# Kernel tuning notes

Measured on AMD Instinct MI355X. Metric: run time of the kernel, lower is better.

## Reference

```python
import jax, jax.numpy as jnp
import numpy as np
import math

BSZ, SEQLEN, DIM = 16, 1, 4096
N_HEADS, N_KV_HEADS = 32, 8
HEAD_DIM = DIM // N_HEADS  # 128
MAX_SEQ_LEN = 4096
START_POS = 4095


def setup_inputs() -> dict:
    key = jax.random.key(0)
    ks = jax.random.split(key, 8)
    w_scale = 0.02
    x = jax.random.normal(ks[0], (1, BSZ, SEQLEN, DIM), jnp.float32)
    wq = jax.random.normal(ks[1], (DIM, DIM), jnp.float32) * w_scale
    wk = jax.random.normal(ks[2], (N_KV_HEADS * HEAD_DIM, DIM), jnp.float32) * w_scale
    wv = jax.random.normal(ks[3], (N_KV_HEADS * HEAD_DIM, DIM), jnp.float32) * w_scale
    wo = jax.random.normal(ks[4], (DIM, DIM), jnp.float32) * w_scale
    cache_k = jax.random.normal(ks[5], (BSZ, MAX_SEQ_LEN, N_KV_HEADS, HEAD_DIM), jnp.float32)
    cache_v = jax.random.normal(ks[6], (BSZ, MAX_SEQ_LEN, N_KV_HEADS, HEAD_DIM), jnp.float32)
    # real RoPE frequencies for positions [START_POS, START_POS+SEQLEN)
    inv_freq = 1.0 / (10000.0 ** (np.arange(0, HEAD_DIM, 2, dtype=np.float32) / HEAD_DIM))
    pos = np.arange(START_POS, START_POS + SEQLEN, dtype=np.float32)
    ang = pos[:, None] * inv_freq[None, :]  # [seqlen, head_dim/2]
    freqs_cos = jnp.asarray(np.cos(ang), jnp.float32)
    freqs_sin = jnp.asarray(np.sin(ang), jnp.float32)
    return {"x": x, "wq": wq, "wk": wk, "wv": wv, "wo": wo,
            "cache_k": cache_k, "cache_v": cache_v,
            "freqs_cos": freqs_cos, "freqs_sin": freqs_sin,
            "start_pos": START_POS}


def _apply_rope(t, cos, sin):
    # t: [b, s, h, d]; cos/sin: [s, d/2]; complex mult over interleaved pairs
    b, s, h, d = t.shape
    tr = t.reshape(b, s, h, d // 2, 2)
    a, bb = tr[..., 0], tr[..., 1]
    c = cos[None, :, None, :]
    sn = sin[None, :, None, :]
    out = jnp.stack([a * c - bb * sn, a * sn + bb * c], axis=-1)
    return out.reshape(b, s, h, d)


def reference(x, wq, wk, wv, wo, cache_k, cache_v, freqs_cos, freqs_sin, start_pos):
    _, bsz, seqlen, dim = x.shape
    n_kv_heads, head_dim = cache_k.shape[2], cache_k.shape[3]
    n_heads = dim // head_dim
    n_rep = n_heads // n_kv_heads

    xq = jnp.einsum('obsd,ed->obse', x, wq).reshape(bsz, seqlen, n_heads, head_dim)
    xk = jnp.einsum('obsd,ed->obse', x, wk).reshape(bsz, seqlen, n_kv_heads, head_dim)
    xv = jnp.einsum('obsd,ed->obse', x, wv).reshape(bsz, seqlen, n_kv_heads, head_dim)

    xq = _apply_rope(xq, freqs_cos, freqs_sin)
    xk = _apply_rope(xk, freqs_cos, freqs_sin)

    cache_k = cache_k.at[:, start_pos:start_pos + seqlen].set(xk)
    cache_v = cache_v.at[:, start_pos:start_pos + seqlen].set(xv)
    keys = cache_k[:, :start_pos + seqlen]    # [b, L, kvh, hd]
    values = cache_v[:, :start_pos + seqlen]

    # repeat_kv (GQA expansion)
    keys = jnp.repeat(keys, n_rep, axis=2)     # [b, L, h, hd]
    values = jnp.repeat(values, n_rep, axis=2)

    scale = 1.0 / math.sqrt(head_dim)
    scores = jnp.einsum('bqhd,bkhd->bhqk', xq, keys) * scale
    # mask is None in decode (seqlen == 1)
    attn = jax.nn.softmax(scores, axis=-1)
    out = jnp.einsum('bhqk,bkhd->bqhd', attn, values)
    out = out.reshape(1, bsz, seqlen, dim)
    return jnp.einsum('obsd,ed->obse', out, wo)
```

## Files before the change

### kernel.cpp

```cpp
#include <hip/hip_runtime.h>
#include <math.h>

#define BSZ 16
#define DIMM 4096
#define NKVH 8
#define HD 128
#define SEQ 4096
#define NSPLIT 16
#define SPLITLEN 256
#define RPAD 65

__device__ __forceinline__ void gll16(const float* src, float* dst) {
  __builtin_amdgcn_global_load_lds(
      (const __attribute__((address_space(1))) void*)src,
      (__attribute__((address_space(3))) void*)dst, 16, 0, 0);
}

__device__ __forceinline__ void stage_chunk(const float* __restrict__ xg,
                                            float* __restrict__ buf, int c,
                                            int wave, int lane) {
#pragma unroll
  for (int u = 0; u < 4; ++u) {
    gll16(xg + (size_t)(u * 4 + wave) * DIMM + c * 256 + (lane << 2),
          buf + u * 1024 + wave * 256);
  }
}

__device__ __forceinline__ void gemv_rows4(const float* __restrict__ xg,
                                           const float* __restrict__ W,
                                           int rbase,
                                           float* __restrict__ x_lds,
                                           float* __restrict__ rbuf,
                                           float res[4], int tid) {
  const int lane = tid & 63;
  const int wave = tid >> 6;
  float acc[4][16];
#pragma unroll
  for (int r = 0; r < 4; ++r)
#pragma unroll
    for (int b = 0; b < 16; ++b) acc[r][b] = 0.f;

  stage_chunk(xg, x_lds, 0, wave, lane);
  float4 w4[4];
#pragma unroll
  for (int r = 0; r < 4; ++r)
    w4[r] = *(const float4*)(W + (size_t)(rbase + r) * DIMM + (lane << 2));

  for (int c = 0; c < 16; ++c) {
    __syncthreads();
    float4 wn[4];
    if (c < 15) {
      stage_chunk(xg, x_lds + ((c + 1) & 1) * 4096, c + 1, wave, lane);
#pragma unroll
      for (int r = 0; r < 4; ++r)
        wn[r] = *(const float4*)(W + (size_t)(rbase + r) * DIMM +
                                 (c + 1) * 256 + (lane << 2));
    }
    const float4* xb = (const float4*)(x_lds + (c & 1) * 4096);
#pragma unroll
    for (int b = 0; b < 16; ++b) {
      float4 xv = xb[b * 64 + lane];
#pragma unroll
      for (int r = 0; r < 4; ++r) {
        acc[r][b] = fmaf(w4[r].x, xv.x, acc[r][b]);
        acc[r][b] = fmaf(w4[r].y, xv.y, acc[r][b]);
        acc[r][b] = fmaf(w4[r].z, xv.z, acc[r][b]);
        acc[r][b] = fmaf(w4[r].w, xv.w, acc[r][b]);
      }
    }
    if (c < 15) {
#pragma unroll
      for (int r = 0; r < 4; ++r) w4[r] = wn[r];
    }
  }

#pragma unroll
  for (int r = 0; r < 4; ++r) {
    __syncthreads();
#pragma unroll
    for (int b = 0; b < 16; ++b) rbuf[b * RPAD + lane] = acc[r][b];
    __syncthreads();
    int bb = lane >> 2, j = lane & 3;
    float s = 0.f;
#pragma unroll
    for (int k = 0; k < 16; ++k) s += rbuf[bb * RPAD + j * 16 + k];
    s += __shfl_xor(s, 1);
    s += __shfl_xor(s, 2);
    res[r] = s;
  }
}

__global__ __launch_bounds__(256) void qkv_kernel(
    const float* __restrict__ x, const float* __restrict__ wq,
    const float* __restrict__ wk, const float* __restrict__ wv,
    const float* __restrict__ fcos, const float* __restrict__ fsin,
    float* __restrict__ q_ws, float* __restrict__ k_ws,
    float* __restrict__ v_ws) {
  __shared__ float x_lds[2 * 4096];
  __shared__ float red[4][16 * RPAD];
  const int tid = threadIdx.x;
  const int lane = tid & 63;
  const int wave = tid >> 6;
  const int row0 = blockIdx.x * 16 + wave * 4;

  const float* W;
  int rbase, kind;
  if (row0 < 4096)      { W = wq; rbase = row0;        kind = 0; }
  else if (row0 < 5120) { W = wk; rbase = row0 - 4096; kind = 1; }
  else                  { W = wv; rbase = row0 - 5120; kind = 2; }

  float res[4];
  gemv_rows4(x, W, rbase, x_lds, red[wave], res, tid);

  if (kind <= 1) {
#pragma unroll
    for (int pr = 0; pr < 2; ++pr) {
      int i = ((rbase + pr * 2) & 127) >> 1;
      float c = fcos[i], s = fsin[i];
      float a = res[pr * 2], b2 = res[pr * 2 + 1];
      res[pr * 2]     = a * c - b2 * s;
      res[pr * 2 + 1] = a * s + b2 * c;
    }
  }
  if ((lane & 3) == 0) {
    int b = lane >> 2;
    if (kind == 0) {
#pragma unroll
      for (int r = 0; r < 4; ++r) q_ws[(size_t)b * 4096 + rbase + r] = res[r];
    } else {
      int kvh = rbase >> 7, dpos = rbase & 127;
      float* dst = (kind == 1) ? k_ws : v_ws;
#pragma unroll
      for (int r = 0; r < 4; ++r)
        dst[((size_t)b * NKVH + kvh) * HD + dpos + r] = res[r];
    }
  }
}

__global__ __launch_bounds__(256) void attn_kernel(
    const float* __restrict__ ck, const float* __restrict__ cv,
    const float* __restrict__ q_ws, const float* __restrict__ k_ws,
    const float* __restrict__ v_ws, float* __restrict__ ml_ws,
    float* __restrict__ opart) {
  __shared__ float sc[SPLITLEN * 4];
  __shared__ float part[32 * 128];
  const int tid = threadIdx.x, lane = tid & 63, wave = tid >> 6;
  const int split = blockIdx.x, kvh = blockIdx.y, b = blockIdx.z;
  const int p0 = split * SPLITLEN;
  const float scale = 0.08838834764831845f;

  {
    const int dsub = (lane & 7) << 2;
    const int prow = lane >> 3;
    float4 q4[4][4];
#pragma unroll
    for (int h = 0; h < 4; ++h)
#pragma unroll
      for (int j = 0; j < 4; ++j) {
        float4 t = *(const float4*)(q_ws + (size_t)b * 4096 + (kvh * 4 + h) * 128 + j * 32 + dsub);
        q4[h][j] = make_float4(t.x * scale, t.y * scale, t.z * scale, t.w * scale);
      }
#pragma unroll 2
    for (int it = 0; it < 8; ++it) {
      int pl = wave * 64 + it * 8 + prow;
      const float* kp = (p0 + pl == SEQ - 1)
                            ? (k_ws + ((size_t)b * NKVH + kvh) * HD)
                            : (ck + ((size_t)(b * 4096 + p0 + pl) * 8 + kvh) * 128);
      float s0 = 0, s1 = 0, s2 = 0, s3 = 0;
#pragma unroll
      for (int j = 0; j < 4; ++j) {
        float4 k4 = *(const float4*)(kp + j * 32 + dsub);
        s0 = fmaf(k4.x, q4[0][j].x, s0); s0 = fmaf(k4.y, q4[0][j].y, s0);
        s0 = fmaf(k4.z, q4[0][j].z, s0); s0 = fmaf(k4.w, q4[0][j].w, s0);
        s1 = fmaf(k4.x, q4[1][j].x, s1); s1 = fmaf(k4.y, q4[1][j].y, s1);
        s1 = fmaf(k4.z, q4[1][j].z, s1); s1 = fmaf(k4.w, q4[1][j].w, s1);
        s2 = fmaf(k4.x, q4[2][j].x, s2); s2 = fmaf(k4.y, q4[2][j].y, s2);
        s2 = fmaf(k4.z, q4[2][j].z, s2); s2 = fmaf(k4.w, q4[2][j].w, s2);
        s3 = fmaf(k4.x, q4[3][j].x, s3); s3 = fmaf(k4.y, q4[3][j].y, s3);
        s3 = fmaf(k4.z, q4[3][j].z, s3); s3 = fmaf(k4.w, q4[3][j].w, s3);
      }
#pragma unroll
      for (int m = 1; m <= 4; m <<= 1) {
        s0 += __shfl_xor(s0, m); s1 += __shfl_xor(s1, m);
        s2 += __shfl_xor(s2, m); s3 += __shfl_xor(s3, m);
      }
      if ((lane & 7) == 0)
        ((float4*)sc)[pl] = make_float4(s0, s1, s2, s3);
    }
  }
  __syncthreads();

  {
    int h = wave;
    float vals[4];
    float m = -1e30f;
#pragma unroll
    for (int k = 0; k < 4; ++k) {
      vals[k] = sc[(k * 64 + lane) * 4 + h];
      m = fmaxf(m, vals[k]);
    }
#pragma unroll
    for (int mk = 1; mk <= 32; mk <<= 1) m = fmaxf(m, __shfl_xor(m, mk));
    float lsum = 0;
#pragma unroll
    for (int k = 0; k < 4; ++k) {
      float e = __expf(vals[k] - m);
      sc[(k * 64 + lane) * 4 + h] = e;
      lsum += e;
    }
#pragma unroll
    for (int mk = 1; mk <= 32; mk <<= 1) lsum += __shfl_xor(lsum, mk);
    if (lane == 0) {
      int hg = kvh * 4 + h;
      ml_ws[((size_t)(b * 32 + hg) * NSPLIT + split) * 2 + 0] = m;
      ml_ws[((size_t)(b * 32 + hg) * NSPLIT + split) * 2 + 1] = lsum;
    }
  }
  __syncthreads();

  {
    const int dq = lane & 31;
    const int half = lane >> 5;
    float4 a0 = {0,0,0,0}, a1 = {0,0,0,0}, a2 = {0,0,0,0}, a3 = {0,0,0,0};
#pragma unroll 4
    for (int it = 0; it < 32; ++it) {
      int pl = wave * 64 + it * 2 + half;
      const float* vp = (p0 + pl == SEQ - 1)
                            ? (v_ws + ((size_t)b * NKVH + kvh) * HD)
                            : (cv + ((size_t)(b * 4096 + p0 + pl) * 8 + kvh) * 128);
      float4 v4 = *(const float4*)(vp + dq * 4);
      float4 s4 = ((const float4*)sc)[pl];
      a0.x = fmaf(s4.x, v4.x, a0.x); a0.y = fmaf(s4.x, v4.y, a0.y);
      a0.z = fmaf(s4.x, v4.z, a0.z); a0.w = fmaf(s4.x, v4.w, a0.w);
      a1.x = fmaf(s4.y, v4.x, a1.x); a1.y = fmaf(s4.y, v4.y, a1.y);
      a1.z = fmaf(s4.y, v4.z, a1.z); a1.w = fmaf(s4.y, v4.w, a1.w);
      a2.x = fmaf(s4.z, v4.x, a2.x); a2.y = fmaf(s4.z, v4.y, a2.y);
      a2.z = fmaf(s4.z, v4.z, a2.z); a2.w = fmaf(s4.z, v4.w, a2.w);
      a3.x = fmaf(s4.w, v4.x, a3.x); a3.y = fmaf(s4.w, v4.y, a3.y);
      a3.z = fmaf(s4.w, v4.z, a3.z); a3.w = fmaf(s4.w, v4.w, a3.w);
    }
    int rb = (half * 16 + wave * 4) * 128 + dq * 4;
    *(float4*)&part[rb + 0 * 128] = a0;
    *(float4*)&part[rb + 1 * 128] = a1;
    *(float4*)&part[rb + 2 * 128] = a2;
    *(float4*)&part[rb + 3 * 128] = a3;
  }
  __syncthreads();
  {
    int hh = tid >> 6, dd = (tid & 63) * 2;
    float o0 = 0, o1 = 0;
#pragma unroll
    for (int g = 0; g < 8; ++g) {
      int row = (g >> 2) * 16 + (g & 3) * 4 + hh;
      float2 p2 = *(const float2*)&part[row * 128 + dd];
      o0 += p2.x; o1 += p2.y;
    }
    int hg = kvh * 4 + hh;
    size_t base = ((size_t)(b * 32 + hg) * NSPLIT + split) * 128;
    *(float2*)(opart + base + dd) = make_float2(o0, o1);
  }
}

__global__ __launch_bounds__(128) void combine_kernel(
    const float* __restrict__ ml_ws, const float* __restrict__ opart,
    float* __restrict__ attn_ws) {
  int bh = blockIdx.x;
  int d = threadIdx.x;
  float mv[NSPLIT], lv[NSPLIT];
  float M = -1e30f;
#pragma unroll
  for (int i = 0; i < NSPLIT; ++i) {
    mv[i] = ml_ws[((size_t)bh * NSPLIT + i) * 2];
    lv[i] = ml_ws[((size_t)bh * NSPLIT + i) * 2 + 1];
    M = fmaxf(M, mv[i]);
  }
  float L = 0, o = 0;
#pragma unroll
  for (int i = 0; i < NSPLIT; ++i) {
    float w = __expf(mv[i] - M);
    L += w * lv[i];
    o += w * opart[((size_t)bh * NSPLIT + i) * 128 + d];
  }
  attn_ws[(size_t)bh * 128 + d] = o / L;
}

__global__ __launch_bounds__(256) void oproj_kernel(
    const float* __restrict__ xin, const float* __restrict__ wo,
    float* __restrict__ out) {
  __shared__ float x_lds[2 * 4096];
  __shared__ float red[4][16 * RPAD];
  const int tid = threadIdx.x;
  const int lane = tid & 63;
  const int wave = tid >> 6;
  const int row0 = blockIdx.x * 16 + wave * 4;
  float res[4];
  gemv_rows4(xin, wo, row0, x_lds, red[wave], res, tid);
  if ((lane & 3) == 0) {
    int b = lane >> 2;
#pragma unroll
    for (int r = 0; r < 4; ++r) out[(size_t)b * 4096 + row0 + r] = res[r];
  }
}

extern "C" void kernel_launch(void* const* d_in, const int* in_sizes, int n_in,
                              void* d_out, int out_size, void* d_ws, size_t ws_size,
                              hipStream_t stream) {
  const float* x  = (const float*)d_in[0];
  const float* wq = (const float*)d_in[1];
  const float* wk = (const float*)d_in[2];
  const float* wv = (const float*)d_in[3];
  const float* wo = (const float*)d_in[4];
  const float* ck = (const float*)d_in[5];
  const float* cv = (const float*)d_in[6];
  const float* fc = (const float*)d_in[7];
  const float* fs = (const float*)d_in[8];

  float* ws      = (float*)d_ws;
  float* q_ws    = ws;
  float* k_ws    = q_ws + 65536;
  float* v_ws    = k_ws + 16384;
  float* ml_ws   = v_ws + 16384;
  float* opart   = ml_ws + 16384;
  float* attn_ws = opart + 1048576;

  qkv_kernel<<<384, 256, 0, stream>>>(x, wq, wk, wv, fc, fs, q_ws, k_ws, v_ws);
  attn_kernel<<<dim3(NSPLIT, NKVH, BSZ), 256, 0, stream>>>(ck, cv, q_ws, k_ws, v_ws,
                                                           ml_ws, opart);
  combine_kernel<<<BSZ * 32, 128, 0, stream>>>(ml_ws, opart, attn_ws);
  oproj_kernel<<<256, 256, 0, stream>>>(attn_ws, wo, (float*)d_out);
}
```

Measured before the change: 632.7 us.

## Drop LDS staging in GEMV, use nontemporal loads, double attention splits

The GEMV helper no longer stages x through LDS with global_load_lds and block barriers. Each wave now reads x directly from global memory, relying on L1/L2 caching, and streams weights with nontemporal loads. The attention kernel doubles the number of splits (NSPLIT 32, SPLITLEN 128) to launch more blocks and uses nontemporal loads for the KV cache; the workspace offsets grow to match. The trade-off is more redundant global reads of x per wave and a larger combine step, in exchange for fewer barriers, no LDS footprint for x, and more parallelism in attention.

Result: faster. 615.2 us (-2.8%).

```diff
diff --git a/kernel.cpp b/kernel.cpp
--- a/kernel.cpp
+++ b/kernel.cpp
@@ -6,67 +6,55 @@
 #define NKVH 8
 #define HD 128
 #define SEQ 4096
-#define NSPLIT 16
-#define SPLITLEN 256
+#define NSPLIT 32
+#define SPLITLEN 128
 #define RPAD 65
 
-__device__ __forceinline__ void gll16(const float* src, float* dst) {
-  __builtin_amdgcn_global_load_lds(
-      (const __attribute__((address_space(1))) void*)src,
-      (__attribute__((address_space(3))) void*)dst, 16, 0, 0);
-}
-
-__device__ __forceinline__ void stage_chunk(const float* __restrict__ xg,
-                                            float* __restrict__ buf, int c,
-                                            int wave, int lane) {
-#pragma unroll
-  for (int u = 0; u < 4; ++u) {
-    gll16(xg + (size_t)(u * 4 + wave) * DIMM + c * 256 + (lane << 2),
-          buf + u * 1024 + wave * 256);
-  }
-}
-
-__device__ __forceinline__ void gemv_rows4(const float* __restrict__ xg,
-                                           const float* __restrict__ W,
-                                           int rbase,
-                                           float* __restrict__ x_lds,
-                                           float* __restrict__ rbuf,
-                                           float res[4], int tid) {
-  const int lane = tid & 63;
-  const int wave = tid >> 6;
+typedef float v4f __attribute__((ext_vector_type(4)));
+
+__device__ __forceinline__ v4f ldg4(const float* p) { return *(const v4f*)p; }
+__device__ __forceinline__ v4f ldnt4(const float* p) {
+  return __builtin_nontemporal_load((const v4f*)p);
+}
+
+__device__ __forceinline__ void gemv4_direct(const float* __restrict__ xg,
+                                             const float* __restrict__ W,
+                                             int rbase,
+                                             float* __restrict__ rbuf,
+                                             float res[4], int lane) {
   float acc[4][16];
 #pragma unroll
   for (int r = 0; r < 4; ++r)
 #pragma unroll
     for (int b = 0; b < 16; ++b) acc[r][b] = 0.f;
 
-  stage_chunk(xg, x_lds, 0, wave, lane);
-  float4 w4[4];
-#pragma unroll
-  for (int r = 0; r < 4; ++r)
-    w4[r] = *(const float4*)(W + (size_t)(rbase + r) * DIMM + (lane << 2));
+  const float* wbase = W + (size_t)rbase * DIMM + (lane << 2);
+  const float* xbase = xg + (lane << 2);
+
+  v4f w4[4];
+#pragma unroll
+  for (int r = 0; r < 4; ++r) w4[r] = ldnt4(wbase + (size_t)r * DIMM);
 
   for (int c = 0; c < 16; ++c) {
-    __syncthreads();
-    float4 wn[4];
+    v4f wn[4];
     if (c < 15) {
-      stage_chunk(xg, x_lds + ((c + 1) & 1) * 4096, c + 1, wave, lane);
 #pragma unroll
       for (int r = 0; r < 4; ++r)
-        wn[r] = *(const float4*)(W + (size_t)(rbase + r) * DIMM +
-                                 (c + 1) * 256 + (lane << 2));
-    }
-    const float4* xb = (const float4*)(x_lds + (c & 1) * 4096);
-#pragma unroll
-    for (int b = 0; b < 16; ++b) {
-      float4 xv = xb[b * 64 + lane];
-#pragma unroll
-      for (int r = 0; r < 4; ++r) {
-        acc[r][b] = fmaf(w4[r].x, xv.x, acc[r][b]);
-        acc[r][b] = fmaf(w4[r].y, xv.y, acc[r][b]);
-        acc[r][b] = fmaf(w4[r].z, xv.z, acc[r][b]);
-        acc[r][b] = fmaf(w4[r].w, xv.w, acc[r][b]);
-      }
+        wn[r] = ldnt4(wbase + (size_t)r * DIMM + (c + 1) * 256);
+    }
+#pragma unroll
+    for (int bh = 0; bh < 2; ++bh) {
+      v4f xv[8];
+#pragma unroll
+      for (int b = 0; b < 8; ++b)
+        xv[b] = ldg4(xbase + (size_t)(bh * 8 + b) * DIMM + c * 256);
+#pragma unroll
+      for (int b = 0; b < 8; ++b)
+#pragma unroll
+        for (int r = 0; r < 4; ++r)
+#pragma unroll
+          for (int e = 0; e < 4; ++e)
+            acc[r][bh * 8 + b] = fmaf(w4[r][e], xv[b][e], acc[r][bh * 8 + b]);
     }
     if (c < 15) {
 #pragma unroll
@@ -76,10 +64,8 @@
 
 #pragma unroll
   for (int r = 0; r < 4; ++r) {
-    __syncthreads();
 #pragma unroll
     for (int b = 0; b < 16; ++b) rbuf[b * RPAD + lane] = acc[r][b];
-    __syncthreads();
     int bb = lane >> 2, j = lane & 3;
     float s = 0.f;
 #pragma unroll
@@ -96,7 +82,6 @@
     const float* __restrict__ fcos, const float* __restrict__ fsin,
     float* __restrict__ q_ws, float* __restrict__ k_ws,
     float* __restrict__ v_ws) {
-  __shared__ float x_lds[2 * 4096];
   __shared__ float red[4][16 * RPAD];
   const int tid = threadIdx.x;
   const int lane = tid & 63;
@@ -110,7 +95,7 @@
   else                  { W = wv; rbase = row0 - 5120; kind = 2; }
 
   float res[4];
-  gemv_rows4(x, W, rbase, x_lds, red[wave], res, tid);
+  gemv4_direct(x, W, rbase, red[wave], res, lane);
 
   if (kind <= 1) {
 #pragma unroll
@@ -161,23 +146,23 @@
         q4[h][j] = make_float4(t.x * scale, t.y * scale, t.z * scale, t.w * scale);
       }
 #pragma unroll 2
-    for (int it = 0; it < 8; ++it) {
-      int pl = wave * 64 + it * 8 + prow;
+    for (int it = 0; it < SPLITLEN / 32; ++it) {
+      int pl = wave * (SPLITLEN / 4) + it * 8 + prow;
       const float* kp = (p0 + pl == SEQ - 1)
                             ? (k_ws + ((size_t)b * NKVH + kvh) * HD)
                             : (ck + ((size_t)(b * 4096 + p0 + pl) * 8 + kvh) * 128);
       float s0 = 0, s1 = 0, s2 = 0, s3 = 0;
 #pragma unroll
       for (int j = 0; j < 4; ++j) {
-        float4 k4 = *(const float4*)(kp + j * 32 + dsub);
-        s0 = fmaf(k4.x, q4[0][j].x, s0); s0 = fmaf(k4.y, q4[0][j].y, s0);
-        s0 = fmaf(k4.z, q4[0][j].z, s0); s0 = fmaf(k4.w, q4[0][j].w, s0);
-        s1 = fmaf(k4.x, q4[1][j].x, s1); s1 = fmaf(k4.y, q4[1][j].y, s1);
-        s1 = fmaf(k4.z, q4[1][j].z, s1); s1 = fmaf(k4.w, q4[1][j].w, s1);
-        s2 = fmaf(k4.x, q4[2][j].x, s2); s2 = fmaf(k4.y, q4[2][j].y, s2);
-        s2 = fmaf(k4.z, q4[2][j].z, s2); s2 = fmaf(k4.w, q4[2][j].w, s2);
-        s3 = fmaf(k4.x, q4[3][j].x, s3); s3 = fmaf(k4.y, q4[3][j].y, s3);
-        s3 = fmaf(k4.z, q4[3][j].z, s3); s3 = fmaf(k4.w, q4[3][j].w, s3);
+        v4f k4 = ldnt4(kp + j * 32 + dsub);
+        s0 = fmaf(k4[0], q4[0][j].x, s0); s0 = fmaf(k4[1], q4[0][j].y, s0);
+        s0 = fmaf(k4[2], q4[0][j].z, s0); s0 = fmaf(k4[3], q4[0][j].w, s0);
+        s1 = fmaf(k4[0], q4[1][j].x, s1); s1 = fmaf(k4[1], q4[1][j].y, s1);
+        s1 = fmaf(k4[2], q4[1][j].z, s1); s1 = fmaf(k4[3], q4[1][j].w, s1);
+        s2 = fmaf(k4[0], q4[2][j].x, s2); s2 = fmaf(k4[1], q4[2][j].y, s2);
+        s2 = fmaf(k4[2], q4[2][j].z, s2); s2 = fmaf(k4[3], q4[2][j].w, s2);
+        s3 = fmaf(k4[0], q4[3][j].x, s3); s3 = fmaf(k4[1], q4[3][j].y, s3);
+        s3 = fmaf(k4[2], q4[3][j].z, s3); s3 = fmaf(k4[3], q4[3][j].w, s3);
       }
 #pragma unroll
       for (int m = 1; m <= 4; m <<= 1) {
@@ -192,10 +177,10 @@
 
   {
     int h = wave;
-    float vals[4];
+    float vals[SPLITLEN / 64];
     float m = -1e30f;
 #pragma unroll
-    for (int k = 0; k < 4; ++k) {
+    for (int k = 0; k < SPLITLEN / 64; ++k) {
       vals[k] = sc[(k * 64 + lane) * 4 + h];
       m = fmaxf(m, vals[k]);
     }
@@ -203,7 +188,7 @@
     for (int mk = 1; mk <= 32; mk <<= 1) m = fmaxf(m, __shfl_xor(m, mk));
     float lsum = 0;
 #pragma unroll
-    for (int k = 0; k < 4; ++k) {
+    for (int k = 0; k < SPLITLEN / 64; ++k) {
       float e = __expf(vals[k] - m);
       sc[(k * 64 + lane) * 4 + h] = e;
       lsum += e;
@@ -223,21 +208,21 @@
     const int half = lane >> 5;
     float4 a0 = {0,0,0,0}, a1 = {0,0,0,0}, a2 = {0,0,0,0}, a3 = {0,0,0,0};
 #pragma unroll 4
-    for (int it = 0; it < 32; ++it) {
-      int pl = wave * 64 + it * 2 + half;
+    for (int it = 0; it < SPLITLEN / 8; ++it) {
+      int pl = wave * (SPLITLEN / 4) + it * 2 + half;
       const float* vp = (p0 + pl == SEQ - 1)
                             ? (v_ws + ((size_t)b * NKVH + kvh) * HD)
                             : (cv + ((size_t)(b * 4096 + p0 + pl) * 8 + kvh) * 128);
-      float4 v4 = *(const float4*)(vp + dq * 4);
+      v4f v4 = ldnt4(vp + dq * 4);
       float4 s4 = ((const float4*)sc)[pl];
-      a0.x = fmaf(s4.x, v4.x, a0.x); a0.y = fmaf(s4.x, v4.y, a0.y);
-      a0.z = fmaf(s4.x, v4.z, a0.z); a0.w = fmaf(s4.x, v4.w, a0.w);
-      a1.x = fmaf(s4.y, v4.x, a1.x); a1.y = fmaf(s4.y, v4.y, a1.y);
-      a1.z = fmaf(s4.y, v4.z, a1.z); a1.w = fmaf(s4.y, v4.w, a1.w);
-      a2.x = fmaf(s4.z, v4.x, a2.x); a2.y = fmaf(s4.z, v4.y, a2.y);
-      a2.z = fmaf(s4.z, v4.z, a2.z); a2.w = fmaf(s4.z, v4.w, a2.w);
-      a3.x = fmaf(s4.w, v4.x, a3.x); a3.y = fmaf(s4.w, v4.y, a3.y);
-      a3.z = fmaf(s4.w, v4.z, a3.z); a3.w = fmaf(s4.w, v4.w, a3.w);
+      a0.x = fmaf(s4.x, v4[0], a0.x); a0.y = fmaf(s4.x, v4[1], a0.y);
+      a0.z = fmaf(s4.x, v4[2], a0.z); a0.w = fmaf(s4.x, v4[3], a0.w);
+      a1.x = fmaf(s4.y, v4[0], a1.x); a1.y = fmaf(s4.y, v4[1], a1.y);
+      a1.z = fmaf(s4.y, v4[2], a1.z); a1.w = fmaf(s4.y, v4[3], a1.w);
+      a2.x = fmaf(s4.z, v4[0], a2.x); a2.y = fmaf(s4.z, v4[1], a2.y);
+      a2.z = fmaf(s4.z, v4[2], a2.z); a2.w = fmaf(s4.z, v4[3], a2.w);
+      a3.x = fmaf(s4.w, v4[0], a3.x); a3.y = fmaf(s4.w, v4[1], a3.y);
+      a3.z = fmaf(s4.w, v4[2], a3.z); a3.w = fmaf(s4.w, v4[3], a3.w);
     }
     int rb = (half * 16 + wave * 4) * 128 + dq * 4;
     *(float4*)&part[rb + 0 * 128] = a0;
@@ -287,14 +272,13 @@
 __global__ __launch_bounds__(256) void oproj_kernel(
     const float* __restrict__ xin, const float* __restrict__ wo,
     float* __restrict__ out) {
-  __shared__ float x_lds[2 * 4096];
   __shared__ float red[4][16 * RPAD];
   const int tid = threadIdx.x;
   const int lane = tid & 63;
   const int wave = tid >> 6;
   const int row0 = blockIdx.x * 16 + wave * 4;
   float res[4];
-  gemv_rows4(xin, wo, row0, x_lds, red[wave], res, tid);
+  gemv4_direct(xin, wo, row0, red[wave], res, lane);
   if ((lane & 3) == 0) {
     int b = lane >> 2;
 #pragma unroll
@@ -320,8 +304,8 @@
   float* k_ws    = q_ws + 65536;
   float* v_ws    = k_ws + 16384;
   float* ml_ws   = v_ws + 16384;
-  float* opart   = ml_ws + 16384;
-  float* attn_ws = opart + 1048576;
+  float* opart   = ml_ws + 32768;
+  float* attn_ws = opart + 2097152;
 
   qkv_kernel<<<384, 256, 0, stream>>>(x, wq, wk, wv, fc, fs, q_ws, k_ws, v_ws);
   attn_kernel<<<dim3(NSPLIT, NKVH, BSZ), 256, 0, stream>>>(ck, cv, q_ws, k_ws, v_ws,
```
